# Optimization experiments

Measured on AMD Instinct MI355X. Metric: run time of the kernel, lower is better.

The kernel has to match this reference:

```python
import jax, jax.numpy as jnp
import numpy as np


def setup_inputs() -> dict:
    key = jax.random.key(0)
    ks = jax.random.split(key, 5)
    B, S, D, F = 4, 2048, 1024, 4096
    scale_w1 = 1.0 / np.sqrt(D)
    scale_w2 = 1.0 / np.sqrt(F)
    return {
        "hidden_states": jax.random.normal(ks[0], (B, S, D), dtype=jnp.float32),
        "W1": jax.random.normal(ks[1], (F, D), dtype=jnp.float32) * scale_w1,
        "b1": jax.random.normal(ks[2], (F,), dtype=jnp.float32) * 0.02,
        "W2": jax.random.normal(ks[3], (D, F), dtype=jnp.float32) * scale_w2,
        "b2": jax.random.normal(ks[4], (D,), dtype=jnp.float32) * 0.02,
    }


def _sigmoid_poly(h):
    # cubic polynomial sigmoid approximation: 0.5 + 0.25*h - 0.0208*h^3
    h2 = h * h
    h3 = h2 * h
    return 0.5 + 0.25 * h + (-0.0208) * h3


def reference(hidden_states, W1, b1, W2, b2):
    # secure linear projection == plain affine: x @ W.T + b
    h = jnp.einsum("bsd,fd->bsf", hidden_states, W1) + b1  # [B,S,F]
    sw = h * _sigmoid_poly(h)                               # swish via poly sigmoid
    out = jnp.einsum("bsf,df->bsd", sw, W2) + b2            # [B,S,D]
    return out
```

## Files before the change

kernel.cpp:

```cpp
#include <hip/hip_runtime.h>
#include <hip/hip_bf16.h>

typedef __bf16 bf16_t;
typedef __bf16 bf16x8 __attribute__((ext_vector_type(8)));
typedef float f32x4 __attribute__((ext_vector_type(4)));

__global__ __launch_bounds__(256) void cast3_f32_to_bf16(
    const float* __restrict__ a, bf16_t* __restrict__ ao, int na8,
    const float* __restrict__ b, bf16_t* __restrict__ bo, int nb8,
    const float* __restrict__ c, bf16_t* __restrict__ co, int nc8) {
  int i = blockIdx.x * blockDim.x + threadIdx.x;
  const float* in;
  bf16_t* out;
  int j;
  if (i < na8) {
    in = a; out = ao; j = i;
  } else if (i < na8 + nb8) {
    in = b; out = bo; j = i - na8;
  } else if (i < na8 + nb8 + nc8) {
    in = c; out = co; j = i - na8 - nb8;
  } else {
    return;
  }
  const float4* in4 = (const float4*)in;
  float4 f0 = in4[2 * j];
  float4 f1 = in4[2 * j + 1];
  bf16x8 o;
  o[0] = (bf16_t)f0.x; o[1] = (bf16_t)f0.y;
  o[2] = (bf16_t)f0.z; o[3] = (bf16_t)f0.w;
  o[4] = (bf16_t)f1.x; o[5] = (bf16_t)f1.y;
  o[6] = (bf16_t)f1.z; o[7] = (bf16_t)f1.w;
  ((bf16x8*)out)[j] = o;
}

__device__ __forceinline__ void gload_lds16(const bf16_t* g, bf16_t* l) {
  __builtin_amdgcn_global_load_lds(
      (const __attribute__((address_space(1))) void*)g,
      (__attribute__((address_space(3))) void*)l,
      16, 0, 0);
}

template <bool SWISH>
__global__ __launch_bounds__(256) void gemm_bt(
    const bf16_t* __restrict__ A, const bf16_t* __restrict__ B,
    const float* __restrict__ bias, void* __restrict__ Cout,
    int M, int N, int K, int XW, int px, int py) {
  const int tid  = threadIdx.x;
  const int wave = tid >> 6;
  const int lane = tid & 63;

  const int bid = blockIdx.x;
  const int xcd = bid & 7;
  const int idx = bid >> 3;
  const int cx = xcd % XW;
  const int cy = xcd / XW;
  const int bx = cx * px + idx % px;
  const int by = cy * py + idx / px;
  const int tileM = by << 7;
  const int tileN = bx << 7;

  __shared__ __align__(16) bf16_t sA[128 * 64];
  __shared__ __align__(16) bf16_t sB[128 * 64];

  const int srow = (wave << 3) + (lane >> 3);
  const int gcol = (((lane & 7) ^ (lane >> 3)) << 3);
  const bf16_t* gA = A + (size_t)(tileM + srow) * K + gcol;
  const bf16_t* gB = B + (size_t)(tileN + srow) * K + gcol;
  bf16_t* lA = sA + (size_t)(wave << 3) * 64;
  bf16_t* lB = sB + (size_t)(wave << 3) * 64;

  const int wr = wave >> 1;
  const int wc = wave & 1;
  const int fRow = lane & 15;
  const int c0 = lane >> 4;
  const int swz = lane & 7;
  const int p0 = c0 ^ swz;
  const int d1 = (((p0 ^ 4) - p0) << 3);
  const bf16x8* pA[4];
  const bf16x8* pB[4];
#pragma unroll
  for (int i = 0; i < 4; ++i) {
    const int lrA = wr * 64 + i * 16 + fRow;
    const int lrB = wc * 64 + i * 16 + fRow;
    pA[i] = (const bf16x8*)(sA + lrA * 64 + p0 * 8);
    pB[i] = (const bf16x8*)(sB + lrB * 64 + p0 * 8);
  }

  f32x4 acc[4][4] = {};

  for (int kt = 0; kt < K; kt += 64) {
#pragma unroll
    for (int r = 0; r < 4; ++r) {
      gload_lds16(gA + kt + (size_t)(r * 32) * K, lA + r * 32 * 64);
      gload_lds16(gB + kt + (size_t)(r * 32) * K, lB + r * 32 * 64);
    }
    __syncthreads();

    bf16x8 a0[4], b0[4];
#pragma unroll
    for (int i = 0; i < 4; ++i) {
      a0[i] = *pA[i];
      b0[i] = *pB[i];
    }
#pragma unroll
    for (int i = 0; i < 4; ++i)
#pragma unroll
      for (int j = 0; j < 4; ++j)
        acc[i][j] = __builtin_amdgcn_mfma_f32_16x16x32_bf16(
            a0[i], b0[j], acc[i][j], 0, 0, 0);

    bf16x8 a1[4], b1[4];
#pragma unroll
    for (int i = 0; i < 4; ++i) {
      a1[i] = *(const bf16x8*)((const bf16_t*)pA[i] + d1);
      b1[i] = *(const bf16x8*)((const bf16_t*)pB[i] + d1);
    }
#pragma unroll
    for (int i = 0; i < 4; ++i)
#pragma unroll
      for (int j = 0; j < 4; ++j)
        acc[i][j] = __builtin_amdgcn_mfma_f32_16x16x32_bf16(
            a1[i], b1[j], acc[i][j], 0, 0, 0);
    __syncthreads();
  }

  const int cRow0 = tileM + wr * 64 + ((lane >> 4) << 2);
  const int cCol0 = tileN + wc * 64 + (lane & 15);
#pragma unroll
  for (int j = 0; j < 4; ++j) {
    const int col = cCol0 + j * 16;
    const float bv = bias[col];
#pragma unroll
    for (int i = 0; i < 4; ++i) {
      const int row = cRow0 + i * 16;
#pragma unroll
      for (int r = 0; r < 4; ++r) {
        float h = acc[i][j][r] + bv;
        if constexpr (SWISH) {
          float h3 = h * h * h;
          float sw = h * (0.5f + 0.25f * h - 0.0208f * h3);
          ((bf16_t*)Cout)[(size_t)(row + r) * N + col] = (bf16_t)sw;
        } else {
          ((float*)Cout)[(size_t)(row + r) * N + col] = h;
        }
      }
    }
  }
}

extern "C" void kernel_launch(void* const* d_in, const int* in_sizes, int n_in,
                              void* d_out, int out_size, void* d_ws,
                              size_t ws_size, hipStream_t stream) {
  const float* X  = (const float*)d_in[0];
  const float* W1 = (const float*)d_in[1];
  const float* b1 = (const float*)d_in[2];
  const float* W2 = (const float*)d_in[3];
  const float* b2 = (const float*)d_in[4];
  float* out = (float*)d_out;

  const int F = in_sizes[2];
  const int D = in_sizes[4];
  const int M = in_sizes[0] / D;

  bf16_t* Xb  = (bf16_t*)d_ws;
  bf16_t* W1b = Xb + (size_t)M * D;
  bf16_t* W2b = W1b + (size_t)F * D;
  bf16_t* SW  = W2b + (size_t)D * F;

  const int nX = (M * D) / 8, nW1 = (F * D) / 8, nW2 = (D * F) / 8;
  const int nTot = nX + nW1 + nW2;
  cast3_f32_to_bf16<<<(nTot + 255) / 256, 256, 0, stream>>>(
      X, Xb, nX, W1, W1b, nW1, W2, W2b, nW2);

  {
    const int gx = F / 128, gy = M / 128;
    const int XW = 2, XH = 4;
    const int px = gx / XW, py = gy / XH;
    gemm_bt<true><<<gx * gy, 256, 0, stream>>>(
        Xb, W1b, b1, (void*)SW, M, F, D, XW, px, py);
  }

  {
    const int gx = D / 128, gy = M / 128;
    const int XW = 1, XH = 8;
    const int px = gx / XW, py = gy / XH;
    gemm_bt<false><<<gx * gy, 256, 0, stream>>>(
        SW, W2b, b2, (void*)out, M, D, F, XW, px, py);
  }
}
```

Before: 268.3 us.

## Replace GEMM with 8-wave 256-row tile kernel using 4-stage LDS pipeline

Replaces the 128x128 single-buffered GEMM with a 512-thread kernel that uses 256xBN tiles, a K-step of 32 and a 4-deep LDS ring buffer. Global-to-LDS loads run three stages ahead, with explicit vmcnt waits, split barriers and MFMA priority raising, so memory traffic overlaps compute. The larger tiles raise operand reuse and the pipelining hides load latency. The cost is more LDS per block, hand-written waitcnt logic that must match the number of issued loads, and fewer blocks for the second GEMM.

```diff
diff --git a/kernel.cpp b/kernel.cpp
--- a/kernel.cpp
+++ b/kernel.cpp
@@ -40,12 +40,69 @@
       16, 0, 0);
 }
 
-template <bool SWISH>
-__global__ __launch_bounds__(256) void gemm_bt(
+template <int N>
+__device__ __forceinline__ void vmwait() {
+  if constexpr (N == 3) asm volatile("s_waitcnt vmcnt(3)" ::: "memory");
+  else if constexpr (N == 4) asm volatile("s_waitcnt vmcnt(4)" ::: "memory");
+  else asm volatile("s_waitcnt vmcnt(0)" ::: "memory");
+}
+
+#define SMALL_TILE(s_, b_, ODD_)                                              \
+  {                                                                           \
+    const int s__ = (s_);                                                     \
+    int sw__ = s__ + 3;                                                       \
+    if (sw__ >= NS) sw__ -= NS;                                               \
+    const bf16_t* bufA = sA + (b_) * (256 * 32);                              \
+    const bf16_t* bufB = sB + (b_) * (BN * 32);                               \
+    bf16x8 af[FRH], bq[FC];                                                   \
+    _Pragma("unroll") for (int i = 0; i < FRH; ++i)                           \
+        af[i] = *(const bf16x8*)(bufA + aoff + i * 512);                      \
+    _Pragma("unroll") for (int j = 0; j < FC; ++j)                            \
+        bq[j] = *(const bf16x8*)(bufB + boff + j * 512);                      \
+    stageA(sw__);                                                             \
+    __builtin_amdgcn_s_barrier();                                             \
+    asm volatile("s_waitcnt lgkmcnt(0)" ::: "memory");                        \
+    __builtin_amdgcn_sched_barrier(0);                                        \
+    __builtin_amdgcn_s_setprio(1);                                            \
+    _Pragma("unroll") for (int i = 0; i < FRH; ++i)                           \
+        _Pragma("unroll") for (int j = 0; j < FC; ++j)                        \
+            acc[i][j] = __builtin_amdgcn_mfma_f32_16x16x32_bf16(              \
+                af[i], bq[j], acc[i][j], 0, 0, 0);                            \
+    __builtin_amdgcn_s_setprio(0);                                            \
+    __builtin_amdgcn_s_barrier();                                             \
+    bf16x8 ag[FRH];                                                           \
+    _Pragma("unroll") for (int i = 0; i < FRH; ++i)                           \
+        ag[i] = *(const bf16x8*)(bufA + aoff + (FRH + i) * 512);              \
+    stageB(sw__);                                                             \
+    __builtin_amdgcn_s_barrier();                                             \
+    asm volatile("s_waitcnt lgkmcnt(0)" ::: "memory");                        \
+    __builtin_amdgcn_sched_barrier(0);                                        \
+    __builtin_amdgcn_s_setprio(1);                                            \
+    _Pragma("unroll") for (int i = 0; i < FRH; ++i)                           \
+        _Pragma("unroll") for (int j = 0; j < FC; ++j)                        \
+            acc[FRH + i][j] = __builtin_amdgcn_mfma_f32_16x16x32_bf16(        \
+                ag[i], bq[j], acc[FRH + i][j], 0, 0, 0);                      \
+    __builtin_amdgcn_s_setprio(0);                                            \
+    if (ODD_) { vmwait<VMN>(); }                                              \
+    __builtin_amdgcn_s_barrier();                                             \
+  }
+
+template <int BN, int WM, int WN, bool SWISH>
+__global__ __launch_bounds__(512, 2) void gemm_bt8(
     const bf16_t* __restrict__ A, const bf16_t* __restrict__ B,
     const float* __restrict__ bias, void* __restrict__ Cout,
     int M, int N, int K, int XW, int px, int py) {
-  const int tid  = threadIdx.x;
+  constexpr int BM = 256;
+  constexpr int WR = BM / WM;
+  constexpr int WC = BN / WN;
+  constexpr int FR = WR / 16;
+  constexpr int FC = WC / 16;
+  constexpr int FRH = FR / 2;
+  constexpr int ACALLS = BM / 128;
+  constexpr int BCALLS = BN / 128;
+  constexpr int VMN = ACALLS + BCALLS;
+
+  const int tid = threadIdx.x;
   const int wave = tid >> 6;
   const int lane = tid & 63;
 
@@ -56,82 +113,66 @@
   const int cy = xcd / XW;
   const int bx = cx * px + idx % px;
   const int by = cy * py + idx / px;
-  const int tileM = by << 7;
-  const int tileN = bx << 7;
-
-  __shared__ __align__(16) bf16_t sA[128 * 64];
-  __shared__ __align__(16) bf16_t sB[128 * 64];
-
-  const int srow = (wave << 3) + (lane >> 3);
-  const int gcol = (((lane & 7) ^ (lane >> 3)) << 3);
-  const bf16_t* gA = A + (size_t)(tileM + srow) * K + gcol;
-  const bf16_t* gB = B + (size_t)(tileN + srow) * K + gcol;
-  bf16_t* lA = sA + (size_t)(wave << 3) * 64;
-  bf16_t* lB = sB + (size_t)(wave << 3) * 64;
-
-  const int wr = wave >> 1;
-  const int wc = wave & 1;
-  const int fRow = lane & 15;
-  const int c0 = lane >> 4;
-  const int swz = lane & 7;
-  const int p0 = c0 ^ swz;
-  const int d1 = (((p0 ^ 4) - p0) << 3);
-  const bf16x8* pA[4];
-  const bf16x8* pB[4];
-#pragma unroll
-  for (int i = 0; i < 4; ++i) {
-    const int lrA = wr * 64 + i * 16 + fRow;
-    const int lrB = wc * 64 + i * 16 + fRow;
-    pA[i] = (const bf16x8*)(sA + lrA * 64 + p0 * 8);
-    pB[i] = (const bf16x8*)(sB + lrB * 64 + p0 * 8);
-  }
-
-  f32x4 acc[4][4] = {};
-
-  for (int kt = 0; kt < K; kt += 64) {
-#pragma unroll
-    for (int r = 0; r < 4; ++r) {
-      gload_lds16(gA + kt + (size_t)(r * 32) * K, lA + r * 32 * 64);
-      gload_lds16(gB + kt + (size_t)(r * 32) * K, lB + r * 32 * 64);
-    }
-    __syncthreads();
-
-    bf16x8 a0[4], b0[4];
-#pragma unroll
-    for (int i = 0; i < 4; ++i) {
-      a0[i] = *pA[i];
-      b0[i] = *pB[i];
-    }
-#pragma unroll
-    for (int i = 0; i < 4; ++i)
-#pragma unroll
-      for (int j = 0; j < 4; ++j)
-        acc[i][j] = __builtin_amdgcn_mfma_f32_16x16x32_bf16(
-            a0[i], b0[j], acc[i][j], 0, 0, 0);
-
-    bf16x8 a1[4], b1[4];
-#pragma unroll
-    for (int i = 0; i < 4; ++i) {
-      a1[i] = *(const bf16x8*)((const bf16_t*)pA[i] + d1);
-      b1[i] = *(const bf16x8*)((const bf16_t*)pB[i] + d1);
-    }
-#pragma unroll
-    for (int i = 0; i < 4; ++i)
-#pragma unroll
-      for (int j = 0; j < 4; ++j)
-        acc[i][j] = __builtin_amdgcn_mfma_f32_16x16x32_bf16(
-            a1[i], b1[j], acc[i][j], 0, 0, 0);
-    __syncthreads();
-  }
-
-  const int cRow0 = tileM + wr * 64 + ((lane >> 4) << 2);
-  const int cCol0 = tileN + wc * 64 + (lane & 15);
-#pragma unroll
-  for (int j = 0; j < 4; ++j) {
+  const int tileM = by * BM;
+  const int tileN = bx * BN;
+
+  __shared__ __align__(16) bf16_t sA[4 * 256 * 32];
+  __shared__ __align__(16) bf16_t sB[4 * BN * 32];
+
+  const int srow = (wave << 4) + (lane >> 2);
+  const int sgc = ((lane & 3) ^ ((lane >> 3) & 3)) << 3;
+  const bf16_t* gA = A + (size_t)(tileM + srow) * K + sgc;
+  const bf16_t* gB = B + (size_t)(tileN + srow) * K + sgc;
+  bf16_t* lA = sA + (wave << 9);
+  bf16_t* lB = sB + (wave << 9);
+
+  auto stageA = [&](int s) {
+    bf16_t* l = lA + (s & 3) * (256 * 32);
+    const bf16_t* g = gA + s * 32;
+#pragma unroll
+    for (int c = 0; c < ACALLS; ++c)
+      gload_lds16(g + (size_t)(c * 128) * K, l + c * 128 * 32);
+  };
+  auto stageB = [&](int s) {
+    bf16_t* l = lB + (s & 3) * (BN * 32);
+    const bf16_t* g = gB + s * 32;
+#pragma unroll
+    for (int c = 0; c < BCALLS; ++c)
+      gload_lds16(g + (size_t)(c * 128) * K, l + c * 128 * 32);
+  };
+
+  const int wr = wave / WN;
+  const int wc = wave % WN;
+  const int fr = lane & 15;
+  const int pc = (lane >> 4) ^ ((fr >> 1) & 3);
+  const int aoff = (wr * WR + fr) * 32 + pc * 8;
+  const int boff = (wc * WC + fr) * 32 + pc * 8;
+
+  f32x4 acc[FR][FC] = {};
+
+  const int NS = K >> 5;
+
+  stageA(0); stageB(0);
+  stageA(1); stageB(1);
+  stageA(2); stageB(2);
+  vmwait<VMN>();
+  __builtin_amdgcn_s_barrier();
+
+  for (int os = 0; os < NS; os += 4) {
+    SMALL_TILE(os + 0, 0, 0)
+    SMALL_TILE(os + 1, 1, 1)
+    SMALL_TILE(os + 2, 2, 0)
+    SMALL_TILE(os + 3, 3, 1)
+  }
+
+  const int cRow0 = tileM + wr * WR + ((lane >> 4) << 2);
+  const int cCol0 = tileN + wc * WC + (lane & 15);
+#pragma unroll
+  for (int j = 0; j < FC; ++j) {
     const int col = cCol0 + j * 16;
     const float bv = bias[col];
 #pragma unroll
-    for (int i = 0; i < 4; ++i) {
+    for (int i = 0; i < FR; ++i) {
       const int row = cRow0 + i * 16;
 #pragma unroll
       for (int r = 0; r < 4; ++r) {
@@ -173,18 +214,18 @@
       X, Xb, nX, W1, W1b, nW1, W2, W2b, nW2);
 
   {
-    const int gx = F / 128, gy = M / 128;
+    const int gx = F / 256, gy = M / 256;
     const int XW = 2, XH = 4;
     const int px = gx / XW, py = gy / XH;
-    gemm_bt<true><<<gx * gy, 256, 0, stream>>>(
+    gemm_bt8<256, 2, 4, true><<<gx * gy, 512, 0, stream>>>(
         Xb, W1b, b1, (void*)SW, M, F, D, XW, px, py);
   }
 
   {
-    const int gx = D / 128, gy = M / 128;
+    const int gx = D / 128, gy = M / 256;
     const int XW = 1, XH = 8;
     const int px = gx / XW, py = gy / XH;
-    gemm_bt<false><<<gx * gy, 256, 0, stream>>>(
+    gemm_bt8<128, 4, 2, false><<<gx * gy, 512, 0, stream>>>(
         SW, W2b, b2, (void*)out, M, D, F, XW, px, py);
   }
 }
```

Result: slower. 274.6 us (+2.3%).
